# Kernel optimization log

Hardware: AMD Instinct MI355X
Metric: run time of the kernel (lower is better)

Reference implementation:

```python
import jax, jax.numpy as jnp
import numpy as np

K = 5
MIN_VAR = 0.001
DUR_SCALE = 1.0
PITCH_SCALE = 1.0
HALF_LOG_2PI_3 = 1.5 * float(np.log(2.0 * np.pi))


def setup_inputs() -> dict:
    key = jax.random.key(0)
    ks = jax.random.split(key, 8)
    B, T, F, N = 16, 1024, 80, 256
    return {
        "mel_out": jax.random.normal(ks[0], (B, T, F * K * 10), dtype=jnp.float32),
        "dec_mask": jnp.ones((B, T, 1), dtype=bool),
        "dur_pred": jax.random.uniform(ks[1], (B, N), dtype=jnp.float32),
        "log_dur_pred": jax.random.normal(ks[2], (B, N), dtype=jnp.float32),
        "pitch_pred": jax.random.normal(ks[3], (B, N), dtype=jnp.float32),
        "mel_tgt": jax.random.normal(ks[4], (B, F, T), dtype=jnp.float32),
        "dur_tgt": jax.random.randint(ks[5], (B, N), 0, 20, dtype=jnp.int64) if jax.config.jax_enable_x64 else jax.random.randint(ks[5], (B, N), 0, 20, dtype=jnp.int32),
        "dur_lens": jax.random.randint(ks[6], (B,), 1, N, dtype=jnp.int32),
        "pitch_tgt": jax.random.normal(ks[7], (B, N), dtype=jnp.float32),
    }


def _mixture_log_prob(p, y):
    # p: (B,T,F,K,10) raw params; y: (B,T,F,3) multivariate targets
    log_w = jax.nn.log_softmax(p[..., 0], axis=-1)          # (B,T,F,K)
    mu = p[..., 1:4]                                         # (B,T,F,K,3)
    diag = jax.nn.softplus(p[..., 4:7]) + MIN_VAR            # L diagonal
    l10 = p[..., 7]
    l21 = p[..., 8]
    l20 = p[..., 9]
    d = y[..., None, :] - mu                                 # (B,T,F,K,3)
    # analytic forward solve of lower-triangular 3x3 system L z = d
    z0 = d[..., 0] / diag[..., 0]
    z1 = (d[..., 1] - l10 * z0) / diag[..., 1]
    z2 = (d[..., 2] - l20 * z0 - l21 * z1) / diag[..., 2]
    maha = z0 * z0 + z1 * z1 + z2 * z2
    comp_logp = -0.5 * maha - jnp.log(diag).sum(-1) - HALF_LOG_2PI_3
    return jax.nn.logsumexp(log_w + comp_logp, axis=-1)     # (B,T,F)


def reference(mel_out, dec_mask, dur_pred, log_dur_pred, pitch_pred,
              mel_tgt, dur_tgt, dur_lens, pitch_tgt):
    B, nmel, T = mel_tgt.shape
    mel_tgt_t = jnp.transpose(mel_tgt, (0, 2, 1))            # (B,T,F)
    N = dur_tgt.shape[1]

    dur_mask = (jnp.arange(N)[None, :] < dur_lens[:, None]).astype(jnp.float32)
    dm_sum = dur_mask.sum()

    log_dur_tgt = jnp.log(dur_tgt.astype(jnp.float32) + 1.0)
    dur_pred_loss = (jnp.square(log_dur_pred - log_dur_tgt) * dur_mask).sum() / dm_sum

    Tdec = dec_mask.shape[1]
    p = mel_out.reshape(B, T, nmel, K, 10)[:, :Tdec]

    # multivariate targets: (self, next-in-time, next-in-freq), zero-padded at edges
    y0 = mel_tgt_t[:, :Tdec]
    y1 = jnp.pad(mel_tgt_t[:, 1:], ((0, 0), (0, 1), (0, 0)))[:, :Tdec]
    y2 = jnp.pad(mel_tgt_t[:, :, 1:], ((0, 0), (0, 0), (0, 1)))[:, :Tdec]
    y = jnp.stack([y0, y1, y2], axis=-1)                     # (B,Tdec,F,3)

    logp = _mixture_log_prob(p, y)                           # (B,Tdec,F)
    mask = dec_mask[..., 0].astype(jnp.float32)              # (B,Tdec)
    mel_loss = -(logp * mask[:, :, None]).sum() / (mask.sum() * nmel)

    ldiff = pitch_tgt.shape[1] - pitch_pred.shape[1]
    pitch_pred_p = jnp.pad(pitch_pred, ((0, 0), (0, ldiff)))
    pitch_loss = (jnp.square(pitch_tgt - pitch_pred_p) * dur_mask).sum() / dm_sum

    loss = mel_loss + pitch_loss * PITCH_SCALE + dur_pred_loss * DUR_SCALE
    return (loss, mel_loss, dur_pred_loss, pitch_loss)
```

## Files before the change

### kernel.cpp

```cpp
#include <hip/hip_runtime.h>
#include <hip/hip_bf16.h>
#include <math.h>

constexpr int B_ = 16, T_ = 1024, F_ = 80, N_ = 256;
constexpr int NBLK = 4096;
constexpr float MIN_VAR_ = 0.001f;
constexpr float HALF_LOG_2PI_3_ = 2.7568155996140185f;

__device__ __forceinline__ float softplus_f(float x) {
    float e = __expf(-fabsf(x));
    return fmaxf(x, 0.0f) + __logf(1.0f + e);
}

__global__ __launch_bounds__(320, 1) void mel_kernel(
    const float* __restrict__ mel_out,
    const unsigned char* __restrict__ dec_mask,
    const float* __restrict__ mel_tgt,
    float* __restrict__ ws)
{
    __shared__ float lds[4 * 4000];
    __shared__ float wpart[5];

    const int tid = threadIdx.x;
    const int r0 = blockIdx.x * 4;

    const int rl  = tid / 80;
    const int f   = tid - rl * 80;
    const int row = r0 + rl;
    const int b   = row >> 10;
    const int t   = row & 1023;
    const float mask = dec_mask[row] ? 1.0f : 0.0f;

    const float* __restrict__ mt = mel_tgt + ((size_t)(b * 80 + f)) * 1024 + t;
    const float y0 = mt[0];
    const float y1 = (t < 1023) ? mt[1] : 0.0f;
    const float y2 = (f < 79)   ? mt[1024] : 0.0f;

    const float4* __restrict__ src4 =
        reinterpret_cast<const float4*>(mel_out) + (size_t)r0 * 1000;
    float4* l4 = reinterpret_cast<float4*>(lds);
    #pragma unroll
    for (int i = 0; i < 13; ++i) {
        int idx = tid + i * 320;
        if (idx < 4000) l4[idx] = src4[idx];
    }
    __syncthreads();

    const float* __restrict__ pp = &lds[rl * 4000 + f * 50];

    float s[5], wv[5];
    #pragma unroll
    for (int k = 0; k < 5; ++k) {
        const float* q = pp + k * 10;
        float2 c0 = *reinterpret_cast<const float2*>(q + 0);
        float2 c1 = *reinterpret_cast<const float2*>(q + 2);
        float2 c2 = *reinterpret_cast<const float2*>(q + 4);
        float2 c3 = *reinterpret_cast<const float2*>(q + 6);
        float2 c4 = *reinterpret_cast<const float2*>(q + 8);

        float w  = c0.x;
        float d0 = y0 - c0.y;
        float d1 = y1 - c1.x;
        float d2 = y2 - c1.y;

        float dg0 = softplus_f(c2.x) + MIN_VAR_;
        float dg1 = softplus_f(c2.y) + MIN_VAR_;
        float dg2 = softplus_f(c3.x) + MIN_VAR_;
        float l10 = c3.y, l21 = c4.x, l20 = c4.y;

        float z0 = d0 * __builtin_amdgcn_rcpf(dg0);
        float z1 = (d1 - l10 * z0) * __builtin_amdgcn_rcpf(dg1);
        float z2 = (d2 - l20 * z0 - l21 * z1) * __builtin_amdgcn_rcpf(dg2);

        float maha = z0 * z0 + z1 * z1 + z2 * z2;
        float comp = -0.5f * maha - __logf(dg0 * dg1 * dg2) - HALF_LOG_2PI_3_;

        wv[k] = w;
        s[k]  = w + comp;
    }

    float ms = s[0], mw = wv[0];
    #pragma unroll
    for (int k = 1; k < 5; ++k) { ms = fmaxf(ms, s[k]); mw = fmaxf(mw, wv[k]); }
    float es = 0.0f, ew = 0.0f;
    #pragma unroll
    for (int k = 0; k < 5; ++k) {
        es += __expf(s[k] - ms);
        ew += __expf(wv[k] - mw);
    }
    float logp = (ms + __logf(es)) - (mw + __logf(ew));

    float v = logp * mask;
    #pragma unroll
    for (int off = 32; off >= 1; off >>= 1) v += __shfl_xor(v, off);
    const int wid = tid >> 6;
    if ((tid & 63) == 0) wpart[wid] = v;
    __syncthreads();
    if (tid == 0) {
        ws[blockIdx.x] = wpart[0] + wpart[1] + wpart[2] + wpart[3] + wpart[4];
    }
}

__global__ __launch_bounds__(256) void finalize_kernel(
    const unsigned char* __restrict__ dec_mask,
    const float* __restrict__ log_dur_pred,
    const float* __restrict__ pitch_pred,
    const int* __restrict__ dur_tgt,
    const int* __restrict__ dur_lens,
    const float* __restrict__ pitch_tgt,
    const float* __restrict__ partials,
    float* __restrict__ out)
{
    __shared__ float red[5][4];
    const int tid = threadIdx.x;
    float dm = 0.0f, dur = 0.0f, pit = 0.0f, msum = 0.0f, mel = 0.0f;

    for (int i = tid; i < NBLK; i += 256) mel += partials[i];

    for (int i = tid; i < B_ * N_; i += 256) {
        int b = i >> 8;
        int n = i & 255;
        if (n < dur_lens[b]) {
            dm += 1.0f;
            float ldt = __logf((float)dur_tgt[i] + 1.0f);
            float dd  = log_dur_pred[i] - ldt;
            dur += dd * dd;
            float pd  = pitch_tgt[i] - pitch_pred[i];
            pit += pd * pd;
        }
    }
    for (int i = tid; i < B_ * T_; i += 256) msum += dec_mask[i] ? 1.0f : 0.0f;

    #pragma unroll
    for (int off = 32; off >= 1; off >>= 1) {
        dm   += __shfl_xor(dm, off);
        dur  += __shfl_xor(dur, off);
        pit  += __shfl_xor(pit, off);
        msum += __shfl_xor(msum, off);
        mel  += __shfl_xor(mel, off);
    }
    const int wid = tid >> 6;
    if ((tid & 63) == 0) {
        red[0][wid] = dm; red[1][wid] = dur; red[2][wid] = pit;
        red[3][wid] = msum; red[4][wid] = mel;
    }
    __syncthreads();
    if (tid == 0) {
        dm   = red[0][0] + red[0][1] + red[0][2] + red[0][3];
        dur  = red[1][0] + red[1][1] + red[1][2] + red[1][3];
        pit  = red[2][0] + red[2][1] + red[2][2] + red[2][3];
        msum = red[3][0] + red[3][1] + red[3][2] + red[3][3];
        mel  = red[4][0] + red[4][1] + red[4][2] + red[4][3];

        float mel_loss   = -mel / (msum * (float)F_);
        float dur_loss   = dur / dm;
        float pitch_loss = pit / dm;
        out[0] = mel_loss + pitch_loss * 1.0f  + dur_loss * 1.0f ;
        out[1] = mel_loss;
        out[2] = dur_loss;
        out[3] = pitch_loss;
    }
}

extern "C" void kernel_launch(void* const* d_in, const int* in_sizes, int n_in,
                              void* d_out, int out_size, void* d_ws, size_t ws_size,
                              hipStream_t stream) {
    const float*         mel_out      = (const float*)d_in[0];
    const unsigned char* dec_mask     = (const unsigned char*)d_in[1];
    const float*         log_dur_pred = (const float*)d_in[3];
    const float*         pitch_pred   = (const float*)d_in[4];
    const float*         mel_tgt      = (const float*)d_in[5];
    const int*           dur_tgt      = (const int*)d_in[6];
    const int*           dur_lens     = (const int*)d_in[7];
    const float*         pitch_tgt    = (const float*)d_in[8];
    float*               ws           = (float*)d_ws;

    mel_kernel<<<dim3(NBLK), dim3(320), 0, stream>>>(mel_out, dec_mask, mel_tgt, ws);

    finalize_kernel<<<dim3(1), dim3(256), 0, stream>>>(
        dec_mask, log_dur_pred, pitch_pred, dur_tgt, dur_lens, pitch_tgt,
        ws, (float*)d_out);
}
```

Baseline: 425.4 us.

## Persistent double-buffered mel kernel with async global-to-LDS loads

The mel kernel becomes a 256-block grid where each block handles 64 rows in 16 groups of four. The mel_out parameters are streamed with global_load_lds into a double buffer so the next group's load overlaps the current group's compute. The mel_tgt slice and mask are staged once per block in LDS, which coalesces the transposed target reads. This trades the old per-block one-shot load for fewer resident blocks, larger LDS use (about 153KB per block), and hand-placed waitcnt and barriers that must be right for correctness.

After: 407.7 us. 1.04x faster.

```diff
diff --git a/kernel.cpp b/kernel.cpp
--- a/kernel.cpp
+++ b/kernel.cpp
@@ -1,9 +1,12 @@
 #include <hip/hip_runtime.h>
-#include <hip/hip_bf16.h>
 #include <math.h>
 
 constexpr int B_ = 16, T_ = 1024, F_ = 80, N_ = 256;
-constexpr int NBLK = 4096;
+constexpr int GRID_MEL = 256;
+constexpr int ROWS_PER_BLOCK = 64;
+constexpr int GROUPS = 16;
+constexpr int SLOTS = 13;
+constexpr long long TOTAL_F4 = 16384LL * 1000;
 constexpr float MIN_VAR_ = 0.001f;
 constexpr float HALF_LOG_2PI_3_ = 2.7568155996140185f;
 
@@ -12,89 +15,130 @@
     return fmaxf(x, 0.0f) + __logf(1.0f + e);
 }
 
-__global__ __launch_bounds__(320, 1) void mel_kernel(
+__device__ __forceinline__ void gload_lds16(const float* g, float* l) {
+    __builtin_amdgcn_global_load_lds(
+        (const __attribute__((address_space(1))) void*)g,
+        (__attribute__((address_space(3))) void*)l,
+        16, 0, 0);
+}
+
+__global__ __launch_bounds__(320) void mel_kernel(
     const float* __restrict__ mel_out,
     const unsigned char* __restrict__ dec_mask,
     const float* __restrict__ mel_tgt,
     float* __restrict__ ws)
 {
-    __shared__ float lds[4 * 4000];
+    __shared__ float buf[2][65 * 256];
+    __shared__ float lds_y[80 * 65];
+    __shared__ float lds_mask[64];
     __shared__ float wpart[5];
 
-    const int tid = threadIdx.x;
-    const int r0 = blockIdx.x * 4;
-
-    const int rl  = tid / 80;
-    const int f   = tid - rl * 80;
-    const int row = r0 + rl;
-    const int b   = row >> 10;
-    const int t   = row & 1023;
-    const float mask = dec_mask[row] ? 1.0f : 0.0f;
-
-    const float* __restrict__ mt = mel_tgt + ((size_t)(b * 80 + f)) * 1024 + t;
-    const float y0 = mt[0];
-    const float y1 = (t < 1023) ? mt[1] : 0.0f;
-    const float y2 = (f < 79)   ? mt[1024] : 0.0f;
-
-    const float4* __restrict__ src4 =
-        reinterpret_cast<const float4*>(mel_out) + (size_t)r0 * 1000;
-    float4* l4 = reinterpret_cast<float4*>(lds);
+    const int tid  = threadIdx.x;
+    const int wave = tid >> 6;
+    const int lane = tid & 63;
+    const int R0   = blockIdx.x * ROWS_PER_BLOCK;
+    const int bb   = R0 >> 10;
+    const int t0   = R0 & 1023;
+
+    {
+        const long long gb = (long long)R0 * 1000;
+        #pragma unroll
+        for (int i = 0; i < SLOTS; ++i) {
+            int c = wave + 5 * i;
+            long long g4 = gb + (long long)c * 64;
+            if (g4 > TOTAL_F4 - 64) g4 = TOTAL_F4 - 64;
+            gload_lds16(mel_out + (g4 + lane) * 4, &buf[0][c * 256]);
+        }
+    }
+
+    for (int idx = tid; idx < 80 * 65; idx += 320) {
+        int f = idx / 65, j = idx - f * 65;
+        int t = t0 + j;
+        lds_y[idx] = (t < 1024) ? mel_tgt[(((long long)(bb * 80 + f)) << 10) + t] : 0.0f;
+    }
+    if (tid < 64) lds_mask[tid] = dec_mask[R0 + tid] ? 1.0f : 0.0f;
+
+    __syncthreads();
+
+    const int rl = tid / 80;
+    const int f  = tid - rl * 80;
+
+    float acc = 0.0f;
+
+    for (int g = 0; g < GROUPS; ++g) {
+        const int nb = g & 1;
+        if (g + 1 < GROUPS) {
+            const long long gb = (long long)(R0 + (g + 1) * 4) * 1000;
+            #pragma unroll
+            for (int i = 0; i < SLOTS; ++i) {
+                int c = wave + 5 * i;
+                long long g4 = gb + (long long)c * 64;
+                if (g4 > TOTAL_F4 - 64) g4 = TOTAL_F4 - 64;
+                gload_lds16(mel_out + (g4 + lane) * 4, &buf[nb ^ 1][c * 256]);
+            }
+            asm volatile("s_waitcnt vmcnt(13)" ::: "memory");
+        } else {
+            asm volatile("s_waitcnt vmcnt(0)" ::: "memory");
+        }
+        __builtin_amdgcn_sched_barrier(0);
+        __builtin_amdgcn_s_barrier();
+        asm volatile("" ::: "memory");
+
+        const int row_loc = g * 4 + rl;
+        const float mask = lds_mask[row_loc];
+        const float y0 = lds_y[f * 65 + row_loc];
+        const float y1 = lds_y[f * 65 + row_loc + 1];
+        const float y2 = (f < 79) ? lds_y[(f + 1) * 65 + row_loc] : 0.0f;
+        const float* pp = &buf[nb][rl * 4000 + f * 50];
+
+        float s[5], wv[5];
+        #pragma unroll
+        for (int k = 0; k < 5; ++k) {
+            const float* q = pp + k * 10;
+            float2 c0 = *reinterpret_cast<const float2*>(q + 0);
+            float2 c1 = *reinterpret_cast<const float2*>(q + 2);
+            float2 c2 = *reinterpret_cast<const float2*>(q + 4);
+            float2 c3 = *reinterpret_cast<const float2*>(q + 6);
+            float2 c4 = *reinterpret_cast<const float2*>(q + 8);
+
+            float w  = c0.x;
+            float d0 = y0 - c0.y;
+            float d1 = y1 - c1.x;
+            float d2 = y2 - c1.y;
+
+            float dg0 = softplus_f(c2.x) + MIN_VAR_;
+            float dg1 = softplus_f(c2.y) + MIN_VAR_;
+            float dg2 = softplus_f(c3.x) + MIN_VAR_;
+
+            float z0 = d0 * __builtin_amdgcn_rcpf(dg0);
+            float z1 = (d1 - c3.y * z0) * __builtin_amdgcn_rcpf(dg1);
+            float z2 = (d2 - c4.y * z0 - c4.x * z1) * __builtin_amdgcn_rcpf(dg2);
+
+            float maha = z0 * z0 + z1 * z1 + z2 * z2;
+            wv[k] = w;
+            s[k]  = w - 0.5f * maha - __logf(dg0 * dg1 * dg2) - HALF_LOG_2PI_3_;
+        }
+
+        float ms = s[0], mw = wv[0];
+        #pragma unroll
+        for (int k = 1; k < 5; ++k) { ms = fmaxf(ms, s[k]); mw = fmaxf(mw, wv[k]); }
+        float es = 0.0f, ew = 0.0f;
+        #pragma unroll
+        for (int k = 0; k < 5; ++k) {
+            es += __expf(s[k] - ms);
+            ew += __expf(wv[k] - mw);
+        }
+        float logp = (ms + __logf(es)) - (mw + __logf(ew));
+        acc += logp * mask;
+
+        asm volatile("" ::: "memory");
+        __builtin_amdgcn_sched_barrier(0);
+        __builtin_amdgcn_s_barrier();
+    }
+
     #pragma unroll
-    for (int i = 0; i < 13; ++i) {
-        int idx = tid + i * 320;
-        if (idx < 4000) l4[idx] = src4[idx];
-    }
-    __syncthreads();
-
-    const float* __restrict__ pp = &lds[rl * 4000 + f * 50];
-
-    float s[5], wv[5];
-    #pragma unroll
-    for (int k = 0; k < 5; ++k) {
-        const float* q = pp + k * 10;
-        float2 c0 = *reinterpret_cast<const float2*>(q + 0);
-        float2 c1 = *reinterpret_cast<const float2*>(q + 2);
-        float2 c2 = *reinterpret_cast<const float2*>(q + 4);
-        float2 c3 = *reinterpret_cast<const float2*>(q + 6);
-        float2 c4 = *reinterpret_cast<const float2*>(q + 8);
-
-        float w  = c0.x;
-        float d0 = y0 - c0.y;
-        float d1 = y1 - c1.x;
-        float d2 = y2 - c1.y;
-
-        float dg0 = softplus_f(c2.x) + MIN_VAR_;
-        float dg1 = softplus_f(c2.y) + MIN_VAR_;
-        float dg2 = softplus_f(c3.x) + MIN_VAR_;
-        float l10 = c3.y, l21 = c4.x, l20 = c4.y;
-
-        float z0 = d0 * __builtin_amdgcn_rcpf(dg0);
-        float z1 = (d1 - l10 * z0) * __builtin_amdgcn_rcpf(dg1);
-        float z2 = (d2 - l20 * z0 - l21 * z1) * __builtin_amdgcn_rcpf(dg2);
-
-        float maha = z0 * z0 + z1 * z1 + z2 * z2;
-        float comp = -0.5f * maha - __logf(dg0 * dg1 * dg2) - HALF_LOG_2PI_3_;
-
-        wv[k] = w;
-        s[k]  = w + comp;
-    }
-
-    float ms = s[0], mw = wv[0];
-    #pragma unroll
-    for (int k = 1; k < 5; ++k) { ms = fmaxf(ms, s[k]); mw = fmaxf(mw, wv[k]); }
-    float es = 0.0f, ew = 0.0f;
-    #pragma unroll
-    for (int k = 0; k < 5; ++k) {
-        es += __expf(s[k] - ms);
-        ew += __expf(wv[k] - mw);
-    }
-    float logp = (ms + __logf(es)) - (mw + __logf(ew));
-
-    float v = logp * mask;
-    #pragma unroll
-    for (int off = 32; off >= 1; off >>= 1) v += __shfl_xor(v, off);
-    const int wid = tid >> 6;
-    if ((tid & 63) == 0) wpart[wid] = v;
+    for (int off = 32; off >= 1; off >>= 1) acc += __shfl_xor(acc, off);
+    if (lane == 0) wpart[wave] = acc;
     __syncthreads();
     if (tid == 0) {
         ws[blockIdx.x] = wpart[0] + wpart[1] + wpart[2] + wpart[3] + wpart[4];
@@ -115,7 +159,7 @@
     const int tid = threadIdx.x;
     float dm = 0.0f, dur = 0.0f, pit = 0.0f, msum = 0.0f, mel = 0.0f;
 
-    for (int i = tid; i < NBLK; i += 256) mel += partials[i];
+    for (int i = tid; i < GRID_MEL; i += 256) mel += partials[i];
 
     for (int i = tid; i < B_ * N_; i += 256) {
         int b = i >> 8;
@@ -175,7 +219,7 @@
     const float*         pitch_tgt    = (const float*)d_in[8];
     float*               ws           = (float*)d_ws;
 
-    mel_kernel<<<dim3(NBLK), dim3(320), 0, stream>>>(mel_out, dec_mask, mel_tgt, ws);
+    mel_kernel<<<dim3(GRID_MEL), dim3(320), 0, stream>>>(mel_out, dec_mask, mel_tgt, ws);
 
     finalize_kernel<<<dim3(1), dim3(256), 0, stream>>>(
         dec_mask, log_dur_pred, pitch_pred, dur_tgt, dur_lens, pitch_tgt,
```
